# Kernel optimization log

Measured on AMD Instinct MI355X. Metric: run time of the kernel, lower is better.

Reference implementation:

```python
import jax, jax.numpy as jnp
import numpy as np

H, DK, DV = 16, 128, 128
BINS = 64
EPS = 1e-6
NORM_EPS = 1e-5


def silu(x):
    return x * jax.nn.sigmoid(x)


def short_conv(x, w):
    # causal depthwise conv over time + silu. x: [B,T,C], w: [C,K]
    C = x.shape[-1]
    K = w.shape[1]
    lhs = jnp.swapaxes(x, 1, 2)              # [B,C,T]
    rhs = w[:, None, :]                      # [C,1,K]
    out = jax.lax.conv_general_dilated(
        lhs, rhs, window_strides=(1,), padding=[(K - 1, 0)],
        dimension_numbers=('NCH', 'OIH', 'NCH'), feature_group_count=C)
    return silu(jnp.swapaxes(out, 1, 2))


def delta_rule(q, k, v, beta, decay):
    # gated delta-rule linear attention recurrence.
    # q,k: [B,T,H,DK], v: [B,T,H,DV], beta: [B,T,H], decay: [B,T,H,DK]
    B = q.shape[0]

    def step(S, inp):
        qt, kt, vt, bt, gt = inp             # [B,H,DK],...,[B,H],[B,H,DK]
        Sd = S * gt[..., None]               # per-key-channel decay
        v_pred = jnp.einsum('bhk,bhkv->bhv', kt, Sd)
        S_new = Sd + jnp.einsum('bhk,bhv->bhkv', kt * bt[..., None], vt - v_pred)
        ot = jnp.einsum('bhk,bhkv->bhv', qt, S_new)
        return S_new, ot

    tm = lambda a: jnp.swapaxes(a, 0, 1)     # time-major
    S0 = jnp.zeros((B, H, DK, DV), q.dtype)
    _, o = jax.lax.scan(step, S0, (tm(q), tm(k), tm(v), tm(beta), tm(decay)))
    return jnp.swapaxes(o, 0, 1)             # [B,T,H,DV]


def _forward(hidden_states, wq, wk, wv, conv_q_w, conv_k_w, conv_v_w, A_log, dt_bias,
             proxy_w, unc_w, head_embed, mlp_w1, mlp_b1, mlp_w2, mlp_b2,
             bb_w, bb_b, bd_w, bd_b, lam_w, lam_b, ab_w, ab_b, ad_w, ad_b,
             g1_w, g2_w, g2_b, onorm_w, wo):
    x = hidden_states
    B, T, _ = x.shape
    q = short_conv(x @ wq, conv_q_w).reshape(B, T, H, DK)
    k = short_conv(x @ wk, conv_k_w).reshape(B, T, H, DK)
    v = short_conv(x @ wv, conv_v_w).reshape(B, T, H, DV)

    # uncertainty (entropy of predicted-token distribution proxy)
    logp = jax.nn.log_softmax(x @ unc_w, axis=-1)
    entropy = -jnp.sum(jnp.exp(logp) * logp, axis=-1)              # [B,T]
    ent_norm = entropy / jnp.log(jnp.asarray(BINS, x.dtype))

    # beta-norm: unit-norm keys inside the kernel
    k_unit = k / (jnp.linalg.norm(k, axis=-1, keepdims=True) + EPS)

    # proxy-value surprise features, per head/token
    v_hat = jnp.einsum('bthk,kv->bthv', k, proxy_w)
    err = v - v_hat
    err_n = jnp.linalg.norm(err, axis=-1)                          # [B,T,H]
    v_n = jnp.linalg.norm(v, axis=-1)
    vh_n = jnp.linalg.norm(v_hat, axis=-1)
    rel_err = err_n / (v_n + EPS)
    cos = jnp.sum(v * v_hat, axis=-1) / (v_n * vh_n + EPS)
    feats = jnp.stack([jnp.broadcast_to(ent_norm[..., None], err_n.shape),
                       rel_err, cos, jnp.log1p(err_n)], axis=-1)    # [B,T,H,4]
    he = jnp.broadcast_to(head_embed[None, None], (B, T, H, head_embed.shape[-1]))
    feats = jnp.concatenate([feats, he], axis=-1)                   # [B,T,H,8]

    hf = silu(silu(feats @ mlp_w1 + mlp_b1) @ mlp_w2 + mlp_b2)      # [B,T,H,32]
    beta_base = hf @ bb_w + bb_b[0]
    beta_delta = hf @ bd_w + bd_b[0]
    beta_fast = jax.nn.sigmoid(beta_base + beta_delta)              # fast memory: bigger step
    beta_slow = jax.nn.sigmoid(beta_base - beta_delta)              # slow memory: smaller step
    lam = jax.nn.sigmoid(hf @ lam_w + lam_b[0])                     # mixing gate
    amp_base = hf @ ab_w + ab_b[0]
    amp_delta = hf @ ad_w + ad_b[0]
    amp_fast = jax.nn.sigmoid(amp_base + amp_delta)
    amp_slow = jax.nn.sigmoid(amp_base - amp_delta)

    # KDA-style per-key-channel log-decay: g = -exp(A_log) * softplus(dt_bias)
    g_chan = -jnp.exp(A_log)[:, None] * jax.nn.softplus(dt_bias).reshape(H, DK)
    decay_fast = jnp.exp(g_chan[None, None] * amp_fast[..., None])  # [B,T,H,DK]
    decay_slow = jnp.exp(g_chan[None, None] * amp_slow[..., None])

    qs = q * (DK ** -0.5)
    o_fast = delta_rule(qs, k_unit, v, beta_fast, decay_fast)
    o_slow = delta_rule(qs, k_unit, v, beta_slow, decay_slow)
    o = lam[..., None] * o_fast + (1.0 - lam[..., None]) * o_slow   # [B,T,H,DV]

    # gated RMSNorm (sigmoid gate) + output projection
    g = ((x @ g1_w) @ g2_w + g2_b).reshape(B, T, H, DV)
    rms = jnp.sqrt(jnp.mean(o * o, axis=-1, keepdims=True) + NORM_EPS)
    o = (o / rms) * onorm_w * jax.nn.sigmoid(g)
    return o.reshape(B, T, H * DV) @ wo


def setup_inputs() -> dict:
    key = jax.random.key(0)
    ks = jax.random.split(key, 40)
    B, T, D = 2, 256, 2048

    def w(k, shape, fan_in):
        return jax.random.normal(k, shape, jnp.float32) * (fan_in ** -0.5)

    return {
        'hidden_states': jax.random.normal(ks[0], (B, T, D), jnp.float32),
        'wq': w(ks[1], (D, H * DK), D),
        'wk': w(ks[2], (D, H * DK), D),
        'wv': w(ks[3], (D, H * DV), D),
        'conv_q_w': w(ks[4], (H * DK, 4), 4),
        'conv_k_w': w(ks[5], (H * DK, 4), 4),
        'conv_v_w': w(ks[6], (H * DV, 4), 4),
        'A_log': jnp.log(jax.random.uniform(ks[7], (H,), jnp.float32, 1.0, 16.0)),
        'dt_bias': jnp.zeros((H * DK,), jnp.float32),
        'proxy_w': w(ks[8], (DK, DV), DK),
        'unc_w': w(ks[9], (D, BINS), D),
        'head_embed': jax.random.normal(ks[10], (H, 4), jnp.float32),
        'mlp_w1': w(ks[11], (8, 32), 8),
        'mlp_b1': jnp.zeros((32,), jnp.float32),
        'mlp_w2': w(ks[12], (32, 32), 32),
        'mlp_b2': jnp.zeros((32,), jnp.float32),
        'bb_w': w(ks[13], (32,), 32), 'bb_b': jnp.zeros((1,), jnp.float32),
        'bd_w': w(ks[14], (32,), 32), 'bd_b': jnp.zeros((1,), jnp.float32),
        'lam_w': w(ks[15], (32,), 32), 'lam_b': jnp.zeros((1,), jnp.float32),
        'ab_w': w(ks[16], (32,), 32), 'ab_b': jnp.zeros((1,), jnp.float32),
        'ad_w': w(ks[17], (32,), 32), 'ad_b': jnp.zeros((1,), jnp.float32),
        'g1_w': w(ks[18], (D, DV), D),
        'g2_w': w(ks[19], (DV, H * DV), DV),
        'g2_b': jnp.zeros((H * DV,), jnp.float32),
        'onorm_w': jnp.ones((DV,), jnp.float32),
        'wo': w(ks[20], (H * DV, D), H * DV),
    }


def reference(hidden_states, wq, wk, wv, conv_q_w, conv_k_w, conv_v_w, A_log, dt_bias,
              proxy_w, unc_w, head_embed, mlp_w1, mlp_b1, mlp_w2, mlp_b2,
              bb_w, bb_b, bd_w, bd_b, lam_w, lam_b, ab_w, ab_b, ad_w, ad_b,
              g1_w, g2_w, g2_b, onorm_w, wo):
    return _forward(hidden_states, wq, wk, wv, conv_q_w, conv_k_w, conv_v_w, A_log,
                    dt_bias, proxy_w, unc_w, head_embed, mlp_w1, mlp_b1, mlp_w2, mlp_b2,
                    bb_w, bb_b, bd_w, bd_b, lam_w, lam_b, ab_w, ab_b, ad_w, ad_b,
                    g1_w, g2_w, g2_b, onorm_w, wo)
```

## Files before the change

kernel.cpp:

```cpp
#include <hip/hip_runtime.h>
#include <hip/hip_bf16.h>
#include <math.h>

#define H_ 16
#define DK_ 128
#define DV_ 128
#define D_ 2048
#define T_ 256
#define B_ 2
#define BT_ 512

typedef __attribute__((ext_vector_type(8))) short short8v;
typedef __attribute__((ext_vector_type(4))) float float4v;
typedef unsigned short ushort_t;

__device__ __forceinline__ float sigmoidf_(float x){ return 1.f/(1.f+expf(-x)); }
__device__ __forceinline__ float siluf_(float x){ return x/(1.f+expf(-x)); }
__device__ __forceinline__ ushort_t f2bf(float f){
    __hip_bfloat16 h = __float2bfloat16(f);
    return *reinterpret_cast<ushort_t*>(&h);
}
__device__ __forceinline__ int swz(int row, int k){
    return row * 32 + ((((k >> 3) ^ (row & 3)) << 3) | (k & 7));
}

template<int CTRL>
__device__ __forceinline__ float ror_add_(float x){
    return x + __int_as_float(__builtin_amdgcn_update_dpp(
        0, __float_as_int(x), CTRL, 0xF, 0xF, true));
}
__device__ __forceinline__ float rsum16_(float x){
    x = ror_add_<0x121>(x);
    x = ror_add_<0x122>(x);
    x = ror_add_<0x124>(x);
    x = ror_add_<0x128>(x);
    return x;
}

__global__ void cvt_gchan(const float* __restrict__ in, ushort_t* __restrict__ out, int n,
                          const float* __restrict__ A_log, const float* __restrict__ dt_bias,
                          float* __restrict__ gchan)
{
    int bid = blockIdx.x;
    if (bid < 1024) {
        int i = (bid * 256 + threadIdx.x) * 4;
        if (i >= n) return;
        float4 v = *(const float4*)&in[i];
        union { ushort_t s[4]; unsigned long long u; } p;
        p.s[0] = f2bf(v.x); p.s[1] = f2bf(v.y); p.s[2] = f2bf(v.z); p.s[3] = f2bf(v.w);
        *(unsigned long long*)&out[i] = p.u;
    } else {
        int i = (bid - 1024) * 256 + threadIdx.x;
        int h = i >> 7;
        float x = dt_bias[i];
        float sp = (x > 20.f) ? x : log1pf(expf(x));
        gchan[i] = -expf(A_log[h]) * sp * 1.44269504088896f;
    }
}

__device__ __forceinline__ void gemm_core(
    const ushort_t* __restrict__ A, int K,
    const float* __restrict__ W, int Nst, int nloc0,
    float* __restrict__ C, int Cst, int m0, int n0out)
{
    __shared__ ushort_t Asub[2048];
    __shared__ ushort_t Bsub[2048];
    const int tid = threadIdx.x;
    const int wid = tid >> 6, lane = tid & 63;
    const int wr = (wid >> 1) * 32, wc = (wid & 1) * 32;
    const int lr = lane & 15, lk = (lane >> 4) * 8;
    const int rowA = tid >> 2, kqA = tid & 3;
    const int nW = tid & 63, kqW = tid >> 6;

    float4v acc[2][2];
    #pragma unroll
    for (int i = 0; i < 2; ++i)
        #pragma unroll
        for (int j = 0; j < 2; ++j) acc[i][j] = (float4v){0.f, 0.f, 0.f, 0.f};

    short8v aRa, aRb;
    float wRa[8], wRb[8];

#define LOADT(AR, WR, KOFF) do {                                                   \
    AR = *(const short8v*)&A[(size_t)(m0 + rowA) * K + (KOFF) + kqA * 8];          \
    _Pragma("unroll")                                                              \
    for (int r = 0; r < 8; ++r)                                                    \
        WR[r] = W[(size_t)((KOFF) + kqW * 8 + r) * Nst + nloc0 + nW];              \
} while (0)
#define STORET(AR, WR) do {                                                        \
    *(short8v*)&Asub[swz(rowA, kqA * 8)] = AR;                                     \
    union { ushort_t s[8]; short8v v; } pk;                                        \
    _Pragma("unroll")                                                              \
    for (int r = 0; r < 8; ++r) pk.s[r] = f2bf(WR[r]);                             \
    *(short8v*)&Bsub[swz(nW, kqW * 8)] = pk.v;                                     \
} while (0)
#define FRAGMMA() do {                                                             \
    short8v af0 = *(const short8v*)&Asub[swz(wr + lr, lk)];                        \
    short8v af1 = *(const short8v*)&Asub[swz(wr + 16 + lr, lk)];                   \
    short8v bf0 = *(const short8v*)&Bsub[swz(wc + lr, lk)];                        \
    short8v bf1 = *(const short8v*)&Bsub[swz(wc + 16 + lr, lk)];                   \
    acc[0][0] = __builtin_amdgcn_mfma_f32_16x16x32_bf16(af0, bf0, acc[0][0],0,0,0);\
    acc[0][1] = __builtin_amdgcn_mfma_f32_16x16x32_bf16(af0, bf1, acc[0][1],0,0,0);\
    acc[1][0] = __builtin_amdgcn_mfma_f32_16x16x32_bf16(af1, bf0, acc[1][0],0,0,0);\
    acc[1][1] = __builtin_amdgcn_mfma_f32_16x16x32_bf16(af1, bf1, acc[1][1],0,0,0);\
} while (0)

    LOADT(aRa, wRa, 0);
    for (int k0 = 0; k0 < K; k0 += 64) {
        STORET(aRa, wRa);
        __syncthreads();
        if (k0 + 32 < K) LOADT(aRb, wRb, k0 + 32);
        FRAGMMA();
        __syncthreads();
        STORET(aRb, wRb);
        __syncthreads();
        if (k0 + 64 < K) LOADT(aRa, wRa, k0 + 64);
        FRAGMMA();
        __syncthreads();
    }
#undef LOADT
#undef STORET
#undef FRAGMMA
    const int lq = (lane >> 4) * 4;
    #pragma unroll
    for (int mi = 0; mi < 2; ++mi)
        #pragma unroll
        for (int ni = 0; ni < 2; ++ni)
            #pragma unroll
            for (int j = 0; j < 4; ++j)
                C[(size_t)(m0 + wr + mi * 16 + lq + j) * Cst + (n0out + wc + ni * 16 + lr)]
                    = acc[mi][ni][j];
}

__device__ __forceinline__ void gemm_core2(
    const ushort_t* __restrict__ A, int K,
    const float* __restrict__ W, int Nst, int nloc0,
    float* __restrict__ C, int Cst, int m0, int n0out)
{
    __shared__ ushort_t Asub[8192];
    __shared__ ushort_t Bsub[2048];
    const int tid = threadIdx.x;
    const int wid = tid >> 6, lane = tid & 63;
    const int wr = wid * 32;
    const int lr = lane & 15, lk = (lane >> 4) * 8;
    const int rowA = tid >> 2;
    const int kqA  = (tid & 3) * 8;
    const int nW = tid & 63, kqW = (tid >> 6) & 3;
    const bool doW = tid < 256;

    float4v acc[2][4];
    #pragma unroll
    for (int i = 0; i < 2; ++i)
        #pragma unroll
        for (int j = 0; j < 4; ++j) acc[i][j] = (float4v){0.f, 0.f, 0.f, 0.f};

    short8v a0a, a1a, a0b, a1b;
    float wRa[8], wRb[8];

#define LOADT2(A0, A1, WR, KOFF) do {                                              \
    A0 = *(const short8v*)&A[(size_t)(m0 + rowA) * K + (KOFF) + kqA];              \
    A1 = *(const short8v*)&A[(size_t)(m0 + rowA + 128) * K + (KOFF) + kqA];        \
    if (doW) {                                                                     \
        _Pragma("unroll")                                                          \
        for (int r = 0; r < 8; ++r)                                                \
            WR[r] = W[(size_t)((KOFF) + kqW * 8 + r) * Nst + nloc0 + nW];          \
    }                                                                              \
} while (0)
#define STORET2(A0, A1, WR) do {                                                   \
    *(short8v*)&Asub[swz(rowA, kqA)] = A0;                                         \
    *(short8v*)&Asub[swz(rowA + 128, kqA)] = A1;                                   \
    if (doW) {                                                                     \
        union { ushort_t s[8]; short8v v; } pk;                                    \
        _Pragma("unroll")                                                          \
        for (int r = 0; r < 8; ++r) pk.s[r] = f2bf(WR[r]);                         \
        *(short8v*)&Bsub[swz(nW, kqW * 8)] = pk.v;                                 \
    }                                                                              \
} while (0)
#define FRAGMMA2() do {                                                            \
    short8v af0 = *(const short8v*)&Asub[swz(wr + lr, lk)];                        \
    short8v af1 = *(const short8v*)&Asub[swz(wr + 16 + lr, lk)];                   \
    short8v bf0 = *(const short8v*)&Bsub[swz(lr, lk)];                             \
    short8v bf1 = *(const short8v*)&Bsub[swz(16 + lr, lk)];                        \
    short8v bf2 = *(const short8v*)&Bsub[swz(32 + lr, lk)];                        \
    short8v bf3 = *(const short8v*)&Bsub[swz(48 + lr, lk)];                        \
    acc[0][0] = __builtin_amdgcn_mfma_f32_16x16x32_bf16(af0, bf0, acc[0][0],0,0,0);\
    acc[0][1] = __builtin_amdgcn_mfma_f32_16x16x32_bf16(af0, bf1, acc[0][1],0,0,0);\
    acc[0][2] = __builtin_amdgcn_mfma_f32_16x16x32_bf16(af0, bf2, acc[0][2],0,0,0);\
    acc[0][3] = __builtin_amdgcn_mfma_f32_16x16x32_bf16(af0, bf3, acc[0][3],0,0,0);\
    acc[1][0] = __builtin_amdgcn_mfma_f32_16x16x32_bf16(af1, bf0, acc[1][0],0,0,0);\
    acc[1][1] = __builtin_amdgcn_mfma_f32_16x16x32_bf16(af1, bf1, acc[1][1],0,0,0);\
    acc[1][2] = __builtin_amdgcn_mfma_f32_16x16x32_bf16(af1, bf2, acc[1][2],0,0,0);\
    acc[1][3] = __builtin_amdgcn_mfma_f32_16x16x32_bf16(af1, bf3, acc[1][3],0,0,0);\
} while (0)

    LOADT2(a0a, a1a, wRa, 0);
    for (int k0 = 0; k0 < K; k0 += 64) {
        STORET2(a0a, a1a, wRa);
        __syncthreads();
        if (k0 + 32 < K) LOADT2(a0b, a1b, wRb, k0 + 32);
        FRAGMMA2();
        __syncthreads();
        STORET2(a0b, a1b, wRb);
        __syncthreads();
        if (k0 + 64 < K) LOADT2(a0a, a1a, wRa, k0 + 64);
        FRAGMMA2();
        __syncthreads();
    }
#undef LOADT2
#undef STORET2
#undef FRAGMMA2
    const int lq = (lane >> 4) * 4;
    #pragma unroll
    for (int mi = 0; mi < 2; ++mi)
        #pragma unroll
        for (int ni = 0; ni < 4; ++ni)
            #pragma unroll
            for (int j = 0; j < 4; ++j)
                C[(size_t)(m0 + wr + mi * 16 + lq + j) * Cst + (n0out + ni * 16 + lr)]
                    = acc[mi][ni][j];
}

__global__ __launch_bounds__(512) void gemm_proj(const ushort_t* __restrict__ A,
    const float* __restrict__ wq, const float* __restrict__ wk, const float* __restrict__ wv,
    const float* __restrict__ unc, const float* __restrict__ g1, float* __restrict__ C)
{
    int n0 = blockIdx.x * 64, m0 = blockIdx.y * 256;
    const float* W; int nloc, Nst;
    if (n0 < 2048)      { W = wq;  nloc = n0;        Nst = 2048; }
    else if (n0 < 4096) { W = wk;  nloc = n0 - 2048; Nst = 2048; }
    else if (n0 < 6144) { W = wv;  nloc = n0 - 4096; Nst = 2048; }
    else if (n0 < 6208) { W = unc; nloc = n0 - 6144; Nst = 64; }
    else                { W = g1;  nloc = n0 - 6208; Nst = 128; }
    gemm_core2(A, 2048, W, Nst, nloc, C, 6336, m0, n0);
}

__global__ __launch_bounds__(256) void gemm_one(const ushort_t* __restrict__ A,
    const float* __restrict__ W, float* __restrict__ C, int N, int K)
{
    gemm_core(A, K, W, N, blockIdx.x * 64, C, N, blockIdx.y * 64, blockIdx.x * 64);
}

__global__ void conv_fused(const float* __restrict__ Cb,
    const float* __restrict__ wq, const float* __restrict__ wk, const float* __restrict__ wv,
    float* __restrict__ qc, float* __restrict__ kc, float* __restrict__ vc,
    ushort_t* __restrict__ kcb, float qscale)
{
    int c  = blockIdx.x * 256 + threadIdx.x;
    int bt = blockIdx.y;
    int b  = bt / T_, t = bt % T_;
    int which = c >> 11, cloc = c & 2047;
    const float* w = which == 0 ? wq : which == 1 ? wk : wv;
    float* o = which == 0 ? qc : which == 1 ? kc : vc;
    float scale = which == 0 ? qscale : 1.f;
    float acc = 0.f;
    #pragma unroll
    for (int j = 0; j < 4; ++j) {
        int tt = t - 3 + j;
        if (tt >= 0) acc = fmaf(w[cloc * 4 + j], Cb[((size_t)(b * T_ + tt)) * 6336 + c], acc);
    }
    float r = siluf_(acc) * scale;
    o[(size_t)bt * D_ + cloc] = r;
    if (which == 1) kcb[(size_t)bt * D_ + cloc] = f2bf(r);
}

__global__ __launch_bounds__(128) void featsprec_k(
    const float* __restrict__ kc, const float* __restrict__ vc,
    const float* __restrict__ qc,
    const float* __restrict__ vhatA, const float* __restrict__ Cb,
    const float* __restrict__ he, const float* __restrict__ gchan,
    const float* __restrict__ w1, const float* __restrict__ b1,
    const float* __restrict__ w2, const float* __restrict__ b2,
    const float* __restrict__ bbw, const float* __restrict__ bbb,
    const float* __restrict__ bdw, const float* __restrict__ bdb,
    const float* __restrict__ lamw, const float* __restrict__ lamb,
    const float* __restrict__ abw, const float* __restrict__ abb,
    const float* __restrict__ adw, const float* __restrict__ adb,
    float* __restrict__ lm, float* __restrict__ kuA,
    float* __restrict__ dA, float4* __restrict__ scal4A)
{
    int blk = blockIdx.x;
    int h = blk & 15, bt = blk >> 4;
    int b = bt / T_, t = bt % T_;
    int v = threadIdx.x;
    __shared__ float part[2][5];
    __shared__ float tot5[5];
    __shared__ float feats8[8];
    __shared__ float hf1[32];
    __shared__ float hf[32];
    __shared__ float entSh;
    __shared__ float scal5[5];

    if (v < 64) {
        float x = Cb[(size_t)bt * 6336 + 6144 + v];
        float m = x;
        #pragma unroll
        for (int o = 32; o > 0; o >>= 1) m = fmaxf(m, __shfl_xor(m, o));
        float e = expf(x - m);
        float s = e;
        #pragma unroll
        for (int o = 32; o > 0; o >>= 1) s += __shfl_xor(s, o);
        float lp = (x - m) - logf(s);
        float c = -expf(lp) * lp;
        #pragma unroll
        for (int o = 32; o > 0; o >>= 1) c += __shfl_xor(c, o);
        if (v == 0) entSh = c / logf(64.f);
    }

    size_t base = (size_t)bt * D_ + h * 128;
    float kval = kc[base + v];
    float vval = vc[base + v];
    float vhat = vhatA[(size_t)blk * 128 + v];

    float e = vval - vhat;
    float sums[5] = {kval * kval, vval * vval, vhat * vhat, vval * vhat, e * e};
    #pragma unroll
    for (int i = 0; i < 5; ++i) {
        float s = sums[i];
        #pragma unroll
        for (int o = 32; o > 0; o >>= 1) s += __shfl_xor(s, o);
        if ((threadIdx.x & 63) == 0) part[threadIdx.x >> 6][i] = s;
    }
    __syncthreads();
    if (threadIdx.x < 5) tot5[threadIdx.x] = part[0][threadIdx.x] + part[1][threadIdx.x];
    __syncthreads();
    if (threadIdx.x == 0) {
        float k2 = tot5[0], v2 = tot5[1], vh2 = tot5[2], vvh = tot5[3], e2 = tot5[4];
        float knorm = sqrtf(k2);
        float err_n = sqrtf(e2);
        float v_n = sqrtf(v2);
        float vh_n = sqrtf(vh2);
        feats8[0] = entSh;
        feats8[1] = err_n / (v_n + 1e-6f);
        feats8[2] = vvh / (v_n * vh_n + 1e-6f);
        feats8[3] = log1pf(err_n);
        feats8[4] = he[h * 4 + 0];
        feats8[5] = he[h * 4 + 1];
        feats8[6] = he[h * 4 + 2];
        feats8[7] = he[h * 4 + 3];
        scal5[4] = knorm;
    }
    __syncthreads();
    if (threadIdx.x < 32) {
        float a = b1[threadIdx.x];
        #pragma unroll
        for (int j = 0; j < 8; ++j) a = fmaf(feats8[j], w1[j * 32 + threadIdx.x], a);
        hf1[threadIdx.x] = siluf_(a);
    }
    __syncthreads();
    if (threadIdx.x < 32) {
        float a = b2[threadIdx.x];
        #pragma unroll
        for (int j = 0; j < 32; ++j) a = fmaf(hf1[j], w2[j * 32 + threadIdx.x], a);
        hf[threadIdx.x] = siluf_(a);
    }
    __syncthreads();
    if (threadIdx.x == 0) {
        float bb = bbb[0], bd = bdb[0], lv = lamb[0], ab = abb[0], ad = adb[0];
        #pragma unroll
        for (int j = 0; j < 32; ++j) {
            float hj = hf[j];
            bb = fmaf(hj, bbw[j], bb);
            bd = fmaf(hj, bdw[j], bd);
            lv = fmaf(hj, lamw[j], lv);
            ab = fmaf(hj, abw[j], ab);
            ad = fmaf(hj, adw[j], ad);
        }
        scal5[0] = sigmoidf_(bb + bd);
        scal5[1] = sigmoidf_(bb - bd);
        scal5[2] = sigmoidf_(ab + ad);
        scal5[3] = sigmoidf_(ab - ad);
        lm[((size_t)(b * H_ + h)) * T_ + t] = sigmoidf_(lv);
    }
    __syncthreads();

    const float bfv = scal5[0], bsv = scal5[1];
    const float afv = scal5[2], asv = scal5[3], knv = scal5[4];
    const int k = threadIdx.x;
    const int bh = b * 16 + h;
    float gch = gchan[h * 128 + k];
    float kuv = kval / (knv + 1e-6f);
    kuA[((size_t)bh * 256 + t) * 128 + k] = kuv;
    dA[((size_t)bh * 256 + t) * 128 + k]        = exp2f(gch * afv);
    dA[((size_t)(32 + bh) * 256 + t) * 128 + k] = exp2f(gch * asv);
    float pq = qc[base + k] * kuv;
    #pragma unroll
    for (int o = 32; o > 0; o >>= 1) pq += __shfl_xor(pq, o);
    if ((threadIdx.x & 63) == 0) part[threadIdx.x >> 6][0] = pq;
    __syncthreads();
    if (threadIdx.x == 0) {
        float pt = part[0][0] + part[1][0];
        float4 s0; s0.x = afv; s0.y = bfv; s0.z = pt * bfv; s0.w = 0.f;
        float4 s1; s1.x = asv; s1.y = bsv; s1.z = pt * bsv; s1.w = 0.f;
        scal4A[(size_t)bh * 256 + t] = s0;
        scal4A[(size_t)(32 + bh) * 256 + t] = s1;
    }
}

struct OPS { float4 a0, a1, q0, q1, d0, d1; float2 vv, sc2; };

__global__ __launch_bounds__(256) void delta_g2_fused(
    const float* __restrict__ qc, const float* __restrict__ vc,
    const float* __restrict__ kuA, const float* __restrict__ dA,
    const float4* __restrict__ scal4A,
    float* __restrict__ o_fast, float* __restrict__ o_slow,
    const float* __restrict__ Cb, const float* __restrict__ g2w,
    float* __restrict__ graw)
{
    __shared__ __align__(16) char smem[59648];
    const int tid = threadIdx.x;

    if (blockIdx.x >= 256) {
        ushort_t* Asub = (ushort_t*)smem;
        ushort_t* Bsub = (ushort_t*)(smem + 4096);
        const int p2 = blockIdx.x - 256;
        const int m0 = (p2 >> 5) * 64, n0 = (p2 & 31) * 64;
        const int wid = tid >> 6, lane = tid & 63;
        const int wr = (wid >> 1) * 32, wc = (wid & 1) * 32;
        const int lr = lane & 15, lk = (lane >> 4) * 8;
        const int rowA = tid >> 2, kqA = (tid & 3) * 8;
        const int nW = tid & 63, kqW = tid >> 6;

        float4v acc[2][2];
        #pragma unroll
        for (int i = 0; i < 2; ++i)
            #pragma unroll
            for (int j = 0; j < 2; ++j) acc[i][j] = (float4v){0.f, 0.f, 0.f, 0.f};

        for (int k0 = 0; k0 < 128; k0 += 32) {
            const float* asrc = &Cb[(size_t)(m0 + rowA) * 6336 + 6208 + k0 + kqA];
            float4 a4a = *(const float4*)asrc;
            float4 a4b = *(const float4*)(asrc + 4);
            float w8[8];
            #pragma unroll
            for (int r = 0; r < 8; ++r)
                w8[r] = g2w[(size_t)(k0 + kqW * 8 + r) * 2048 + n0 + nW];
            __syncthreads();
            union { ushort_t s[8]; short8v v; } pa, pw;
            pa.s[0]=f2bf(a4a.x); pa.s[1]=f2bf(a4a.y); pa.s[2]=f2bf(a4a.z); pa.s[3]=f2bf(a4a.w);
            pa.s[4]=f2bf(a4b.x); pa.s[5]=f2bf(a4b.y); pa.s[6]=f2bf(a4b.z); pa.s[7]=f2bf(a4b.w);
            *(short8v*)&Asub[swz(rowA, kqA)] = pa.v;
            #pragma unroll
            for (int r = 0; r < 8; ++r) pw.s[r] = f2bf(w8[r]);
            *(short8v*)&Bsub[swz(nW, kqW * 8)] = pw.v;
            __syncthreads();
            short8v af0 = *(const short8v*)&Asub[swz(wr + lr, lk)];
            short8v af1 = *(const short8v*)&Asub[swz(wr + 16 + lr, lk)];
            short8v bf0 = *(const short8v*)&Bsub[swz(wc + lr, lk)];
            short8v bf1 = *(const short8v*)&Bsub[swz(wc + 16 + lr, lk)];
            acc[0][0] = __builtin_amdgcn_mfma_f32_16x16x32_bf16(af0, bf0, acc[0][0],0,0,0);
            acc[0][1] = __builtin_amdgcn_mfma_f32_16x16x32_bf16(af0, bf1, acc[0][1],0,0,0);
            acc[1][0] = __builtin_amdgcn_mfma_f32_16x16x32_bf16(af1, bf0, acc[1][0],0,0,0);
            acc[1][1] = __builtin_amdgcn_mfma_f32_16x16x32_bf16(af1, bf1, acc[1][1],0,0,0);
        }
        const int lq = (lane >> 4) * 4;
        #pragma unroll
        for (int mi = 0; mi < 2; ++mi)
            #pragma unroll
            for (int ni = 0; ni < 2; ++ni)
                #pragma unroll
                for (int j = 0; j < 4; ++j)
                    graw[(size_t)(m0 + wr + mi * 16 + lq + j) * 2048 + (n0 + wc + ni * 16 + lr)]
                        = acc[mi][ni][j];
        return;
    }

    float (*kuL)[16][144] = (float (*)[16][144])(smem);
    float (*qL)[16][144]  = (float (*)[16][144])(smem + 18432);
    float (*dL)[16][144]  = (float (*)[16][144])(smem + 36864);
    float (*vL)[16][32]   = (float (*)[16][32])(smem + 55296);
    float (*scL)[16][2]   = (float (*)[16][2])(smem + 59392);

    const int p  = blockIdx.x;
    const int lb = (p & 7) * 32 + (p >> 3);
    const int bh = lb >> 3, rule = (lb >> 2) & 1, vq = lb & 3;
    const int b = bh >> 4, h = bh & 15;
    const int rbh = rule * 32 + bh;
    const int wid = tid >> 6, lane = tid & 63;
    const int kl = lane & 15, vg = lane >> 4;
    const int vloc = wid * 8 + vg * 2;
    const int vcol = vq * 32 + vloc;

    const float*  __restrict__ pkuG = kuA + (size_t)bh * 256 * 128;
    const float*  __restrict__ pdG  = dA + (size_t)rbh * 256 * 128;
    const float*  __restrict__ pqG  = qc + (size_t)b * T_ * D_ + h * 128;
    const float*  __restrict__ pvG  = vc + (size_t)b * T_ * D_ + h * 128 + vq * 32;
    const float4* __restrict__ pscG = scal4A + (size_t)rbh * 256;
    float* __restrict__ obase = (rule ? o_slow : o_fast)
                                + (size_t)b * T_ * D_ + h * 128 + vcol;

    const int srow = (tid & 127) >> 3;
    const int scol = (tid & 7) * 16;
    const bool isK = tid < 128;
    const int ck0 = scol >> 3;
    const int fo_w0 = ck0 * 8 + (ck0 >> 2) * 4;
    const int fo_w1 = (ck0 + 1) * 8 + ((ck0 + 1) >> 2) * 4;

    float4 sb0, sb1, sb2, sb3, svb, ssc, sd0, sd1;

    float S[8][2];
    #pragma unroll
    for (int j = 0; j < 8; ++j) { S[j][0] = 0.f; S[j][1] = 0.f; }

#define STAGE_LOAD(C) do {                                                         \
    const int t0_ = (C) * 16;                                                      \
    const float* dsrc = pdG + (size_t)(t0_ + srow) * 128 + scol;                   \
    if (isK) {                                                                     \
        const float* src = pkuG + (size_t)(t0_ + srow) * 128 + scol;               \
        sb0 = *(const float4*)(src);      sb1 = *(const float4*)(src + 4);         \
        sb2 = *(const float4*)(src + 8);  sb3 = *(const float4*)(src + 12);        \
        svb = *(const float4*)(pvG + (size_t)(t0_ + srow) * D_ + (tid & 7) * 4);   \
        sd0 = *(const float4*)(dsrc);     sd1 = *(const float4*)(dsrc + 4);        \
    } else {                                                                       \
        const float* src = pqG + (size_t)(t0_ + srow) * D_ + scol;                 \
        sb0 = *(const float4*)(src);      sb1 = *(const float4*)(src + 4);         \
        sb2 = *(const float4*)(src + 8);  sb3 = *(const float4*)(src + 12);        \
        sd0 = *(const float4*)(dsrc + 8); sd1 = *(const float4*)(dsrc + 12);       \
        if ((tid & 127) < 16) ssc = *(const float4*)&pscG[t0_ + (tid & 127)];      \
    }                                                                              \
} while (0)

#define STAGE_WRITE(BI) do {                                                       \
    if (isK) {                                                                     \
        *(float4*)&kuL[BI][srow][fo_w0]     = sb0;                                 \
        *(float4*)&kuL[BI][srow][fo_w0 + 4] = sb1;                                 \
        *(float4*)&kuL[BI][srow][fo_w1]     = sb2;                                 \
        *(float4*)&kuL[BI][srow][fo_w1 + 4] = sb3;                                 \
        *(float4*)&vL[BI][srow][(tid & 7) * 4] = svb;                              \
        *(float4*)&dL[BI][srow][fo_w0]      = sd0;                                 \
        *(float4*)&dL[BI][srow][fo_w0 + 4]  = sd1;                                 \
    } else {                                                                       \
        *(float4*)&qL[BI][srow][fo_w0]     = sb0;                                  \
        *(float4*)&qL[BI][srow][fo_w0 + 4] = sb1;                                  \
        *(float4*)&qL[BI][srow][fo_w1]     = sb2;                                  \
        *(float4*)&qL[BI][srow][fo_w1 + 4] = sb3;                                  \
        *(float4*)&dL[BI][srow][fo_w1]      = sd0;                                 \
        *(float4*)&dL[BI][srow][fo_w1 + 4]  = sd1;                                 \
        if ((tid & 127) < 16) {                                                    \
            float2 w2_; w2_.x = ssc.y; w2_.y = ssc.z;                              \
            *(float2*)&scL[BI][tid & 127][0] = w2_;                                \
        }                                                                          \
    }                                                                              \
} while (0)

#define LDOPS(R, BI, TS) do {                                                      \
    R.a0 = *(const float4*)&kuL[BI][TS][fo];                                       \
    R.a1 = *(const float4*)&kuL[BI][TS][fo + 4];                                   \
    R.q0 = *(const float4*)&qL[BI][TS][fo];                                        \
    R.q1 = *(const float4*)&qL[BI][TS][fo + 4];                                    \
    R.d0 = *(const float4*)&dL[BI][TS][fo];                                        \
    R.d1 = *(const float4*)&dL[BI][TS][fo + 4];                                    \
    R.vv = *(const float2*)&vL[BI][TS][vloc];                                      \
    R.sc2 = *(const float2*)&scL[BI][TS][0];                                       \
} while (0)

#define STEP(TT, CUR, NXT, BI) do {                                                \
    if ((TT) + 1 < 16) LDOPS(NXT, BI, (TT) + 1);                                   \
    float ku[8] = {CUR.a0.x, CUR.a0.y, CUR.a0.z, CUR.a0.w,                         \
                   CUR.a1.x, CUR.a1.y, CUR.a1.z, CUR.a1.w};                        \
    float qv[8] = {CUR.q0.x, CUR.q0.y, CUR.q0.z, CUR.q0.w,                         \
                   CUR.q1.x, CUR.q1.y, CUR.q1.z, CUR.q1.w};                        \
    float d[8]  = {CUR.d0.x, CUR.d0.y, CUR.d0.z, CUR.d0.w,                         \
                   CUR.d1.x, CUR.d1.y, CUR.d1.z, CUR.d1.w};                        \
    float vp0a = 0.f, vp0b = 0.f, vp1a = 0.f, vp1b = 0.f;                          \
    float oq0a = 0.f, oq0b = 0.f, oq1a = 0.f, oq1b = 0.f;                          \
    _Pragma("unroll")                                                              \
    for (int j = 0; j < 4; ++j) {                                                  \
        float kudA = ku[j] * d[j],     qdA = qv[j] * d[j];                         \
        float kudB = ku[j+4] * d[j+4], qdB = qv[j+4] * d[j+4];                     \
        vp0a = fmaf(kudA, S[j][0], vp0a);   vp0b = fmaf(kudB, S[j+4][0], vp0b);    \
        vp1a = fmaf(kudA, S[j][1], vp1a);   vp1b = fmaf(kudB, S[j+4][1], vp1b);    \
        oq0a = fmaf(qdA,  S[j][0], oq0a);   oq0b = fmaf(qdB,  S[j+4][0], oq0b);    \
        oq1a = fmaf(qdA,  S[j][1], oq1a);   oq1b = fmaf(qdB,  S[j+4][1], oq1b);    \
    }                                                                              \
    float vp0 = rsum16_(vp0a + vp0b);                                              \
    float vp1 = rsum16_(vp1a + vp1b);                                              \
    float oq0 = rsum16_(oq0a + oq0b);                                              \
    float oq1 = rsum16_(oq1a + oq1b);                                              \
    float dv0 = CUR.vv.x - vp0, dv1 = CUR.vv.y - vp1;                              \
    float o0 = fmaf(CUR.sc2.y, dv0, oq0);                                          \
    float o1 = fmaf(CUR.sc2.y, dv1, oq1);                                          \
    float bd0 = CUR.sc2.x * dv0, bd1 = CUR.sc2.x * dv1;                            \
    _Pragma("unroll")                                                              \
    for (int j = 0; j < 8; ++j) {                                                  \
        S[j][0] = fmaf(d[j], S[j][0], ku[j] * bd0);                                \
        S[j][1] = fmaf(d[j], S[j][1], ku[j] * bd1);                                \
    }                                                                              \
    if (kl == 0) {                                                                 \
        float2 ov; ov.x = o0; ov.y = o1;                                           \
        *(float2*)&obase[(size_t)(tb + (TT)) * D_] = ov;                           \
    }                                                                              \
} while (0)

    const int fo = kl * 8 + (kl >> 2) * 4;

    STAGE_LOAD(0);
    STAGE_WRITE(0);
    __syncthreads();

    OPS rA, rB;
    for (int c = 0; c < 16; ++c) {
        if (c < 15) STAGE_LOAD(c + 1);
        const int bi = c & 1;
        const int tb = c * 16;
        LDOPS(rA, bi, 0);
        #pragma unroll
        for (int ts = 0; ts < 16; ts += 2) {
            STEP(ts,     rA, rB, bi);
            STEP(ts + 1, rB, rA, bi);
        }
        if (c < 15) STAGE_WRITE((c + 1) & 1);
        __syncthreads();
    }
#undef STAGE_LOAD
#undef STAGE_WRITE
#undef LDOPS
#undef STEP
}

__global__ __launch_bounds__(128) void combine_k(
    const float* __restrict__ of, const float* __restrict__ os,
    const float* __restrict__ lm, const float* __restrict__ graw,
    const float* __restrict__ g2b, const float* __restrict__ onw,
    ushort_t* __restrict__ ocb)
{
    int blk = blockIdx.x;
    int h = blk & 15, bt = blk >> 4;
    int b = bt / T_, t = bt % T_;
    int v = threadIdx.x;
    size_t idx = (size_t)bt * D_ + h * 128 + v;
    float l = lm[((size_t)(b * H_ + h)) * T_ + t];
    float o = l * of[idx] + (1.f - l) * os[idx];
    float s = o * o;
    #pragma unroll
    for (int off = 32; off > 0; off >>= 1) s += __shfl_xor(s, off);
    __shared__ float ws2[2];
    if ((threadIdx.x & 63) == 0) ws2[threadIdx.x >> 6] = s;
    __syncthreads();
    float tot = ws2[0] + ws2[1];
    float rms = sqrtf(tot / 128.f + 1e-5f);
    float g = graw[idx] + g2b[h * 128 + v];
    ocb[idx] = f2bf(o / rms * onw[v] * sigmoidf_(g));
}

extern "C" void kernel_launch(void* const* d_in, const int* in_sizes, int n_in,
                              void* d_out, int out_size, void* d_ws, size_t ws_size,
                              hipStream_t stream)
{
    const float* x        = (const float*)d_in[0];
    const float* wq       = (const float*)d_in[1];
    const float* wk       = (const float*)d_in[2];
    const float* wv       = (const float*)d_in[3];
    const float* conv_q_w = (const float*)d_in[4];
    const float* conv_k_w = (const float*)d_in[5];
    const float* conv_v_w = (const float*)d_in[6];
    const float* A_log    = (const float*)d_in[7];
    const float* dt_bias  = (const float*)d_in[8];
    const float* proxy_w  = (const float*)d_in[9];
    const float* unc_w    = (const float*)d_in[10];
    const float* he       = (const float*)d_in[11];
    const float* mlp_w1   = (const float*)d_in[12];
    const float* mlp_b1   = (const float*)d_in[13];
    const float* mlp_w2   = (const float*)d_in[14];
    const float* mlp_b2   = (const float*)d_in[15];
    const float* bb_w     = (const float*)d_in[16];
    const float* bb_b     = (const float*)d_in[17];
    const float* bd_w     = (const float*)d_in[18];
    const float* bd_b     = (const float*)d_in[19];
    const float* lam_w    = (const float*)d_in[20];
    const float* lam_b    = (const float*)d_in[21];
    const float* ab_w     = (const float*)d_in[22];
    const float* ab_b     = (const float*)d_in[23];
    const float* ad_w     = (const float*)d_in[24];
    const float* ad_b     = (const float*)d_in[25];
    const float* g1_w     = (const float*)d_in[26];
    const float* g2_w     = (const float*)d_in[27];
    const float* g2_b     = (const float*)d_in[28];
    const float* onorm_w  = (const float*)d_in[29];
    const float* wo       = (const float*)d_in[30];
    float* out = (float*)d_out;

    float* ws = (float*)d_ws;
    const size_t SZ = (size_t)BT_ * D_;
    float* C_big = ws;
    float* qc    = C_big + (size_t)512 * 6336;
    float* kc    = qc + SZ;
    float* vc    = kc + SZ;
    float* graw  = vc + SZ;
    float* lm    = graw + SZ;
    float* gchan = lm + 8192;
    float* scal4 = gchan + 2048;
    float* kuA   = scal4 + 65536;
    float* dA    = kuA + 1048576;
    float* vhatA = dA + 2097152;
    float* fend  = vhatA + 1048576;
    ushort_t* xb = (ushort_t*)fend;

    float* o_fast  = kc;
    float* o_slow  = vhatA;
    ushort_t* ocb  = xb;
    ushort_t* kcb  = (ushort_t*)dA;

    dim3 blk256(256);
    dim3 blk512(512);
    const float QSCALE = 0.08838834764831845f;

    cvt_gchan<<<dim3(1032), blk256, 0, stream>>>(x, xb, (int)SZ, A_log, dt_bias, gchan);
    gemm_proj<<<dim3(99, 2), blk512, 0, stream>>>(xb, wq, wk, wv, unc_w, g1_w, C_big);
    conv_fused<<<dim3(24, BT_), blk256, 0, stream>>>(C_big, conv_q_w, conv_k_w, conv_v_w,
                                                     qc, kc, vc, kcb, QSCALE);
    gemm_one<<<dim3(2, 128), blk256, 0, stream>>>(kcb, proxy_w, vhatA, 128, 128);
    featsprec_k<<<dim3(BT_ * H_), dim3(128), 0, stream>>>(
        kc, vc, qc, vhatA, C_big, he, gchan,
        mlp_w1, mlp_b1, mlp_w2, mlp_b2,
        bb_w, bb_b, bd_w, bd_b, lam_w, lam_b, ab_w, ab_b, ad_w, ad_b,
        lm, kuA, dA, (float4*)scal4);
    delta_g2_fused<<<dim3(512), blk256, 0, stream>>>(qc, vc, kuA, dA,
                                                     (const float4*)scal4,
                                                     o_fast, o_slow,
                                                     C_big, g2_w, graw);
    combine_k<<<dim3(BT_ * H_), dim3(128), 0, stream>>>(o_fast, o_slow, lm, graw,
                                                        g2_b, onorm_w, ocb);
    gemm_one<<<dim3(32, 8), blk256, 0, stream>>>(ocb, wo, out, 2048, 2048);
}
```

Baseline: 206.5 us.

## Split delta-rule recurrence across twice as many blocks with one value column per thread

```diff
diff --git a/kernel.cpp b/kernel.cpp
--- a/kernel.cpp
+++ b/kernel.cpp
@@ -396,7 +396,7 @@
     }
 }
 
-struct OPS { float4 a0, a1, q0, q1, d0, d1; float2 vv, sc2; };
+struct OPS { float4 a0, a1, q0, q1, d0, d1; float2 sc2; float vv; };
 
 __global__ __launch_bounds__(256) void delta_g2_fused(
     const float* __restrict__ qc, const float* __restrict__ vc,
@@ -406,13 +406,13 @@
     const float* __restrict__ Cb, const float* __restrict__ g2w,
     float* __restrict__ graw)
 {
-    __shared__ __align__(16) char smem[59648];
+    __shared__ __align__(16) char smem[57600];
     const int tid = threadIdx.x;
 
-    if (blockIdx.x >= 256) {
+    if (blockIdx.x >= 512) {
         ushort_t* Asub = (ushort_t*)smem;
         ushort_t* Bsub = (ushort_t*)(smem + 4096);
-        const int p2 = blockIdx.x - 256;
+        const int p2 = blockIdx.x - 512;
         const int m0 = (p2 >> 5) * 64, n0 = (p2 & 31) * 64;
         const int wid = tid >> 6, lane = tid & 63;
         const int wr = (wid >> 1) * 32, wc = (wid & 1) * 32;
@@ -467,23 +467,23 @@
     float (*kuL)[16][144] = (float (*)[16][144])(smem);
     float (*qL)[16][144]  = (float (*)[16][144])(smem + 18432);
     float (*dL)[16][144]  = (float (*)[16][144])(smem + 36864);
-    float (*vL)[16][32]   = (float (*)[16][32])(smem + 55296);
-    float (*scL)[16][2]   = (float (*)[16][2])(smem + 59392);
+    float (*vL)[16][16]   = (float (*)[16][16])(smem + 55296);
+    float (*scL)[16][2]   = (float (*)[16][2])(smem + 57344);
 
     const int p  = blockIdx.x;
-    const int lb = (p & 7) * 32 + (p >> 3);
-    const int bh = lb >> 3, rule = (lb >> 2) & 1, vq = lb & 3;
+    const int lb = (p & 7) * 64 + (p >> 3);
+    const int bh = lb >> 4, rule = (lb >> 3) & 1, vq = lb & 7;
     const int b = bh >> 4, h = bh & 15;
     const int rbh = rule * 32 + bh;
     const int wid = tid >> 6, lane = tid & 63;
     const int kl = lane & 15, vg = lane >> 4;
-    const int vloc = wid * 8 + vg * 2;
-    const int vcol = vq * 32 + vloc;
+    const int vloc = wid * 4 + vg;
+    const int vcol = vq * 16 + vloc;
 
     const float*  __restrict__ pkuG = kuA + (size_t)bh * 256 * 128;
     const float*  __restrict__ pdG  = dA + (size_t)rbh * 256 * 128;
     const float*  __restrict__ pqG  = qc + (size_t)b * T_ * D_ + h * 128;
-    const float*  __restrict__ pvG  = vc + (size_t)b * T_ * D_ + h * 128 + vq * 32;
+    const float*  __restrict__ pvG  = vc + (size_t)b * T_ * D_ + h * 128 + vq * 16;
     const float4* __restrict__ pscG = scal4A + (size_t)rbh * 256;
     float* __restrict__ obase = (rule ? o_slow : o_fast)
                                 + (size_t)b * T_ * D_ + h * 128 + vcol;
@@ -497,9 +497,9 @@
 
     float4 sb0, sb1, sb2, sb3, svb, ssc, sd0, sd1;
 
-    float S[8][2];
-    #pragma unroll
-    for (int j = 0; j < 8; ++j) { S[j][0] = 0.f; S[j][1] = 0.f; }
+    float S[8];
+    #pragma unroll
+    for (int j = 0; j < 8; ++j) S[j] = 0.f;
 
 #define STAGE_LOAD(C) do {                                                         \
     const int t0_ = (C) * 16;                                                      \
@@ -508,7 +508,8 @@
         const float* src = pkuG + (size_t)(t0_ + srow) * 128 + scol;               \
         sb0 = *(const float4*)(src);      sb1 = *(const float4*)(src + 4);         \
         sb2 = *(const float4*)(src + 8);  sb3 = *(const float4*)(src + 12);        \
-        svb = *(const float4*)(pvG + (size_t)(t0_ + srow) * D_ + (tid & 7) * 4);   \
+        if ((tid & 7) < 4)                                                         \
+            svb = *(const float4*)(pvG + (size_t)(t0_ + srow) * D_ + (tid & 3) * 4);\
         sd0 = *(const float4*)(dsrc);     sd1 = *(const float4*)(dsrc + 4);        \
     } else {                                                                       \
         const float* src = pqG + (size_t)(t0_ + srow) * D_ + scol;                 \
@@ -525,7 +526,7 @@
         *(float4*)&kuL[BI][srow][fo_w0 + 4] = sb1;                                 \
         *(float4*)&kuL[BI][srow][fo_w1]     = sb2;                                 \
         *(float4*)&kuL[BI][srow][fo_w1 + 4] = sb3;                                 \
-        *(float4*)&vL[BI][srow][(tid & 7) * 4] = svb;                              \
+        if ((tid & 7) < 4) *(float4*)&vL[BI][srow][(tid & 3) * 4] = svb;           \
         *(float4*)&dL[BI][srow][fo_w0]      = sd0;                                 \
         *(float4*)&dL[BI][srow][fo_w0 + 4]  = sd1;                                 \
     } else {                                                                       \
@@ -549,7 +550,7 @@
     R.q1 = *(const float4*)&qL[BI][TS][fo + 4];                                    \
     R.d0 = *(const float4*)&dL[BI][TS][fo];                                        \
     R.d1 = *(const float4*)&dL[BI][TS][fo + 4];                                    \
-    R.vv = *(const float2*)&vL[BI][TS][vloc];                                      \
+    R.vv = vL[BI][TS][vloc];                                                       \
     R.sc2 = *(const float2*)&scL[BI][TS][0];                                       \
 } while (0)
 
@@ -561,34 +562,23 @@
                    CUR.q1.x, CUR.q1.y, CUR.q1.z, CUR.q1.w};                        \
     float d[8]  = {CUR.d0.x, CUR.d0.y, CUR.d0.z, CUR.d0.w,                         \
                    CUR.d1.x, CUR.d1.y, CUR.d1.z, CUR.d1.w};                        \
-    float vp0a = 0.f, vp0b = 0.f, vp1a = 0.f, vp1b = 0.f;                          \
-    float oq0a = 0.f, oq0b = 0.f, oq1a = 0.f, oq1b = 0.f;                          \
+    float vpa = 0.f, vpb = 0.f, oqa = 0.f, oqb = 0.f;                              \
     _Pragma("unroll")                                                              \
     for (int j = 0; j < 4; ++j) {                                                  \
         float kudA = ku[j] * d[j],     qdA = qv[j] * d[j];                         \
         float kudB = ku[j+4] * d[j+4], qdB = qv[j+4] * d[j+4];                     \
-        vp0a = fmaf(kudA, S[j][0], vp0a);   vp0b = fmaf(kudB, S[j+4][0], vp0b);    \
-        vp1a = fmaf(kudA, S[j][1], vp1a);   vp1b = fmaf(kudB, S[j+4][1], vp1b);    \
-        oq0a = fmaf(qdA,  S[j][0], oq0a);   oq0b = fmaf(qdB,  S[j+4][0], oq0b);    \
-        oq1a = fmaf(qdA,  S[j][1], oq1a);   oq1b = fmaf(qdB,  S[j+4][1], oq1b);    \
+        vpa = fmaf(kudA, S[j], vpa);   vpb = fmaf(kudB, S[j+4], vpb);              \
+        oqa = fmaf(qdA,  S[j], oqa);   oqb = fmaf(qdB,  S[j+4], oqb);              \
     }                                                                              \
-    float vp0 = rsum16_(vp0a + vp0b);                                              \
-    float vp1 = rsum16_(vp1a + vp1b);                                              \
-    float oq0 = rsum16_(oq0a + oq0b);                                              \
-    float oq1 = rsum16_(oq1a + oq1b);                                              \
-    float dv0 = CUR.vv.x - vp0, dv1 = CUR.vv.y - vp1;                              \
-    float o0 = fmaf(CUR.sc2.y, dv0, oq0);                                          \
-    float o1 = fmaf(CUR.sc2.y, dv1, oq1);                                          \
-    float bd0 = CUR.sc2.x * dv0, bd1 = CUR.sc2.x * dv1;                            \
+    float vp = rsum16_(vpa + vpb);                                                 \
+    float oq = rsum16_(oqa + oqb);                                                 \
+    float dv = CUR.vv - vp;                                                        \
+    float o = fmaf(CUR.sc2.y, dv, oq);                                             \
+    float bd = CUR.sc2.x * dv;                                                     \
     _Pragma("unroll")                                                              \
-    for (int j = 0; j < 8; ++j) {                                                  \
-        S[j][0] = fmaf(d[j], S[j][0], ku[j] * bd0);                                \
-        S[j][1] = fmaf(d[j], S[j][1], ku[j] * bd1);                                \
-    }                                                                              \
-    if (kl == 0) {                                                                 \
-        float2 ov; ov.x = o0; ov.y = o1;                                           \
-        *(float2*)&obase[(size_t)(tb + (TT)) * D_] = ov;                           \
-    }                                                                              \
+    for (int j = 0; j < 8; ++j)                                                    \
+        S[j] = fmaf(d[j], S[j], ku[j] * bd);                                       \
+    if (kl == 0) obase[(size_t)(tb + (TT)) * D_] = o;                              \
 } while (0)
 
     const int fo = kl * 8 + (kl >> 2) * 4;
@@ -714,7 +704,7 @@
         mlp_w1, mlp_b1, mlp_w2, mlp_b2,
         bb_w, bb_b, bd_w, bd_b, lam_w, lam_b, ab_w, ab_b, ad_w, ad_b,
         lm, kuA, dA, (float4*)scal4);
-    delta_g2_fused<<<dim3(512), blk256, 0, stream>>>(qc, vc, kuA, dA,
+    delta_g2_fused<<<dim3(768), blk256, 0, stream>>>(qc, vc, kuA, dA,
                                                      (const float4*)scal4,
                                                      o_fast, o_slow,
                                                      C_big, g2_w, graw);
```

After: 226.8 us. +9.8%, slower.
